# Kernel optimization log

Hardware: AMD Instinct MI355X
Metric: run time of the kernel (lower is better)

Reference implementation:

```python
import math
import jax, jax.numpy as jnp
import numpy as np

L, D, H, F, V, S, B = 6, 1024, 16, 4096, 32000, 1024, 2
DH = D // H


def setup_inputs() -> dict:
    key = jax.random.key(0)
    ks = jax.random.split(key, 24)

    def u(k, shape, fan_in):
        b = 1.0 / math.sqrt(fan_in)
        return jax.random.uniform(k, shape, jnp.float32, -b, b)

    inp = {
        "input_ids": jax.random.randint(ks[0], (B, S), 0, V),
        "attention_mask": jnp.ones((B, 1, 1, S), dtype=bool),
        "emb": jax.random.normal(ks[1], (V, D), jnp.float32),
        "pos": 0.02 * jax.random.normal(ks[2], (1, S, D), jnp.float32),
        "ln1_w": jnp.ones((L, D), jnp.float32),
        "ln1_b": jnp.zeros((L, D), jnp.float32),
        "qw": u(ks[3], (L, D, D), D), "qb": u(ks[4], (L, D), D),
        "kw": u(ks[5], (L, D, D), D), "kb": u(ks[6], (L, D), D),
        "vw": u(ks[7], (L, D, D), D), "vb": u(ks[8], (L, D), D),
        "ow": u(ks[9], (L, D, D), D), "ob": u(ks[10], (L, D), D),
        "ln2_w": jnp.ones((L, D), jnp.float32),
        "ln2_b": jnp.zeros((L, D), jnp.float32),
        "w1": u(ks[11], (L, F, D), D), "b1": u(ks[12], (L, F), D),
        "w2": u(ks[13], (L, D, F), F), "b2": u(ks[14], (L, D), F),
    }
    return inp


def _ln(x, w, b, eps=1e-5):
    m = x.mean(axis=-1, keepdims=True)
    v = ((x - m) ** 2).mean(axis=-1, keepdims=True)  # unbiased=False
    return w * (x - m) / jnp.sqrt(v + eps) + b


def _gelu(x):
    # tanh-approx GELU, exactly as in source
    return 0.5 * x * (1.0 + jnp.tanh(math.sqrt(2.0 / math.pi) * (x + 0.044715 * x ** 3)))


def reference(input_ids, attention_mask, emb, pos, ln1_w, ln1_b,
              qw, qb, kw, kb, vw, vb, ow, ob,
              ln2_w, ln2_b, w1, b1, w2, b2):
    b, s = input_ids.shape
    d = emb.shape[1]
    scale = math.sqrt(DH)
    x = emb[input_ids] * math.sqrt(d) + pos[:, :s, :]  # [B,S,D]
    n_layers = qw.shape[0]
    for l in range(n_layers):
        h = _ln(x, ln1_w[l], ln1_b[l])
        q = (h @ qw[l].T + qb[l]).reshape(b, s, H, DH)
        k = (h @ kw[l].T + kb[l]).reshape(b, s, H, DH)
        v = (h @ vw[l].T + vb[l]).reshape(b, s, H, DH)
        scores = jnp.einsum('bqhd,bkhd->bhqk', q, k) / scale  # [B,H,S,S]
        scores = jnp.where(attention_mask, scores, -jnp.inf)
        attn = jax.nn.softmax(scores, axis=-1)
        o = jnp.einsum('bhqk,bkhd->bqhd', attn, v).reshape(b, s, d)
        x = x + (o @ ow[l].T + ob[l])
        h2 = _ln(x, ln2_w[l], ln2_b[l])
        x = x + (_gelu(h2 @ w1[l].T + b1[l]) @ w2[l].T + b2[l])
    return x
```

## Files before the change

### kernel.cpp

```cpp
#include <hip/hip_runtime.h>
#include <hip/hip_bf16.h>
#include <math.h>

#define D_ 1024
#define H_ 16
#define F_ 4096
#define S_ 1024
#define B_ 2
#define MTOT 2048

using bf16 = __hip_bfloat16;
typedef __bf16 bf16x8 __attribute__((ext_vector_type(8)));
typedef float f32x4 __attribute__((ext_vector_type(4)));

__device__ __forceinline__ void gload_lds16(const void* g, void* l) {
  __builtin_amdgcn_global_load_lds((const __attribute__((address_space(1))) void*)g,
                                   (__attribute__((address_space(3))) void*)l, 16, 0, 0);
}

__device__ __forceinline__ unsigned short f2b(float f) {
  union { bf16 h; unsigned short u; } c;
  c.h = __float2bfloat16(f);
  return c.u;
}

__global__ __launch_bounds__(256) void embed_kernel(const int* __restrict__ ids,
    const float* __restrict__ emb, const float* __restrict__ pos, float* __restrict__ x) {
  int row = blockIdx.x;
  int s = row & (S_ - 1);
  int id = ids[row];
  const float4* e = (const float4*)(emb + (size_t)id * D_);
  const float4* p = (const float4*)(pos + (size_t)s * D_);
  float4* xo = (float4*)(x + (size_t)row * D_);
  int t = threadIdx.x;
  float4 ev = e[t], pv = p[t], r;
  r.x = ev.x * 32.0f + pv.x; r.y = ev.y * 32.0f + pv.y;
  r.z = ev.z * 32.0f + pv.z; r.w = ev.w * 32.0f + pv.w;
  xo[t] = r;
}

__global__ __launch_bounds__(256) void ln_kernel(const float* __restrict__ x,
    const float* __restrict__ w, const float* __restrict__ b, bf16* __restrict__ h) {
  int row = blockIdx.x, t = threadIdx.x;
  const float4* xr = (const float4*)(x + (size_t)row * D_);
  float4 v = xr[t];
  float s = v.x + v.y + v.z + v.w;
  float s2 = v.x * v.x + v.y * v.y + v.z * v.z + v.w * v.w;
  #pragma unroll
  for (int o = 32; o; o >>= 1) { s += __shfl_down(s, o); s2 += __shfl_down(s2, o); }
  __shared__ float red[8];
  int wave = t >> 6, lane = t & 63;
  if (lane == 0) { red[wave] = s; red[4 + wave] = s2; }
  __syncthreads();
  float mean = (red[0] + red[1] + red[2] + red[3]) * (1.0f / D_);
  float m2   = (red[4] + red[5] + red[6] + red[7]) * (1.0f / D_);
  float rstd = rsqrtf(m2 - mean * mean + 1e-5f);
  float4 wv = ((const float4*)w)[t], bv = ((const float4*)b)[t];
  ushort4 o4;
  o4.x = f2b((v.x - mean) * rstd * wv.x + bv.x);
  o4.y = f2b((v.y - mean) * rstd * wv.y + bv.y);
  o4.z = f2b((v.z - mean) * rstd * wv.z + bv.z);
  o4.w = f2b((v.w - mean) * rstd * wv.w + bv.w);
  ((ushort4*)(h + (size_t)row * D_))[t] = o4;
}

__global__ __launch_bounds__(256) void cvt6_kernel(const float4* __restrict__ s0,
    const float4* __restrict__ s1, const float4* __restrict__ s2, const float4* __restrict__ s3,
    const float4* __restrict__ s4, const float4* __restrict__ s5, ushort4* __restrict__ dst) {
  int i = blockIdx.x * 256 + threadIdx.x;
  const float4* src; int off;
  if (i < 1048576) {
    int seg = i >> 18; off = i & 262143;
    src = seg == 0 ? s0 : seg == 1 ? s1 : seg == 2 ? s2 : s3;
  } else if (i < 2097152) { src = s4; off = i - 1048576; }
  else                    { src = s5; off = i - 2097152; }
  float4 v = src[off];
  ushort4 r;
  r.x = f2b(v.x); r.y = f2b(v.y); r.z = f2b(v.z); r.w = f2b(v.w);
  dst[i] = r;
}

template<int MODE>
__global__ __launch_bounds__(256) void gemm_bt(const bf16* __restrict__ A,
    const bf16* __restrict__ Bw,
    const float* __restrict__ b0_, const float* __restrict__ b1_, const float* __restrict__ b2_,
    void* __restrict__ o0, void* __restrict__ o1, void* __restrict__ o2,
    int M, int N, int K, int kspl) {
  __shared__ alignas(16) bf16 As[2][128 * 64];
  __shared__ alignas(16) bf16 Bs[2][128 * 64];
  int tid = threadIdx.x, wave = tid >> 6, lane = tid & 63;
  int nbn = N >> 7;
  int nwg = gridDim.x;
  int bid = blockIdx.x;
  int swz = (bid & 7) * (nwg >> 3) + (bid >> 3);
  int bm = swz / nbn, bn = swz % nbn;
  int m0 = bm << 7, n0 = bn << 7;
  int kbase = blockIdx.z * kspl;
  int wr = wave >> 1, wc = wave & 1;
  int lr = lane & 15, lg = lane >> 4;

  auto stage = [&](int buf, int k0) {
    #pragma unroll
    for (int j = 0; j < 4; j++) {
      int cidx = j * 256 + tid;
      int r = cidx >> 3, s = cidx & 7;
      int g = s ^ (r & 7);
      bf16* abase = &As[buf][(j * 256 + wave * 64) * 8];
      bf16* bbase = &Bs[buf][(j * 256 + wave * 64) * 8];
      gload_lds16(A  + (size_t)(m0 + r) * K + k0 + g * 8, abase);
      gload_lds16(Bw + (size_t)(n0 + r) * K + k0 + g * 8, bbase);
    }
  };

  f32x4 acc[4][4] = {};
  int nk = kspl >> 6;
  stage(0, kbase);
  __syncthreads();
  int cur = 0;
  for (int t = 0; t < nk; ++t) {
    if (t + 1 < nk) stage(cur ^ 1, kbase + (t + 1) * 64);
    __builtin_amdgcn_s_setprio(1);
    #pragma unroll
    for (int kk = 0; kk < 2; ++kk) {
      bf16x8 af[4], bfr[4];
      #pragma unroll
      for (int f = 0; f < 4; f++) {
        int ra = wr * 64 + f * 16 + lr;
        int rb = wc * 64 + f * 16 + lr;
        af[f]  = *(const bf16x8*)&As[cur][ra * 64 + (((kk * 4 + lg) ^ (ra & 7)) * 8)];
        bfr[f] = *(const bf16x8*)&Bs[cur][rb * 64 + (((kk * 4 + lg) ^ (rb & 7)) * 8)];
      }
      #pragma unroll
      for (int mf = 0; mf < 4; mf++)
        #pragma unroll
        for (int nf = 0; nf < 4; nf++)
          acc[mf][nf] = __builtin_amdgcn_mfma_f32_16x16x32_bf16(af[mf], bfr[nf], acc[mf][nf], 0, 0, 0);
    }
    __builtin_amdgcn_s_setprio(0);
    __syncthreads();
    cur ^= 1;
  }

  #pragma unroll
  for (int mf = 0; mf < 4; mf++) {
    #pragma unroll
    for (int nf = 0; nf < 4; nf++) {
      int n = n0 + wc * 64 + nf * 16 + lr;
      if (MODE == 0 && n >= 2048) {
        int nl = n & 1023;
        int mbase = m0 + wr * 64 + mf * 16 + lg * 4;
        int bb = mbase >> 10, sb = mbase & 1023;
        float bias = b2_[nl];
        ushort4 pk;
        pk.x = f2b(acc[mf][nf][0] + bias);
        pk.y = f2b(acc[mf][nf][1] + bias);
        pk.z = f2b(acc[mf][nf][2] + bias);
        pk.w = f2b(acc[mf][nf][3] + bias);
        *(ushort4*)&((bf16*)o2)[((size_t)(bb * 1024 + nl)) * 1024 + sb] = pk;
      } else {
        #pragma unroll
        for (int i = 0; i < 4; i++) {
          int m = m0 + wr * 64 + mf * 16 + lg * 4 + i;
          float v = acc[mf][nf][i];
          if (MODE == 0) {
            int seg = n >> 10, nl = n & 1023;
            if (seg == 0)      ((bf16*)o0)[(size_t)m * 1024 + nl] = __float2bfloat16(v + b0_[nl]);
            else               ((bf16*)o1)[(size_t)m * 1024 + nl] = __float2bfloat16(v + b1_[nl]);
          } else if (MODE == 1) {
            float bias = (blockIdx.z == 0) ? b0_[n] : 0.0f;
            atomicAdd(&((float*)o0)[(size_t)m * N + n], v + bias);
          } else {
            float g = v + b0_[n];
            float t = tanhf(0.7978845608028654f * (g + 0.044715f * g * g * g));
            ((bf16*)o0)[(size_t)m * N + n] = __float2bfloat16(0.5f * g * (1.0f + t));
          }
        }
      }
    }
  }
}

__global__ __launch_bounds__(256) void attn_kernel(const bf16* __restrict__ qbuf,
    const bf16* __restrict__ kbuf, const bf16* __restrict__ vT, bf16* __restrict__ obuf) {
  int bh = blockIdx.y;
  int b = bh >> 4, h = bh & 15;
  int q0 = blockIdx.x * 16;
  int tid = threadIdx.x, wave = tid >> 6, lane = tid & 63;
  int lr = lane & 15, lg = lane >> 4;

  __shared__ alignas(16) bf16 P[16][1032];
  __shared__ float red[4][16];

  const bf16* qp = qbuf + ((size_t)(b * S_ + q0)) * D_ + h * 64;
  bf16x8 aq[2];
  aq[0] = *(const bf16x8*)(qp + (size_t)lr * D_ + lg * 8);
  aq[1] = *(const bf16x8*)(qp + (size_t)lr * D_ + 32 + lg * 8);

  const bf16* kb_ = kbuf + ((size_t)(b * S_)) * D_ + h * 64;
  int nbase = wave * 256;
  f32x4 acc[16] = {};
  #pragma unroll
  for (int nf = 0; nf < 16; nf++) {
    const bf16* kp = kb_ + (size_t)(nbase + nf * 16 + lr) * D_ + lg * 8;
    bf16x8 bk0 = *(const bf16x8*)(kp);
    bf16x8 bk1 = *(const bf16x8*)(kp + 32);
    acc[nf] = __builtin_amdgcn_mfma_f32_16x16x32_bf16(aq[0], bk0, acc[nf], 0, 0, 0);
    acc[nf] = __builtin_amdgcn_mfma_f32_16x16x32_bf16(aq[1], bk1, acc[nf], 0, 0, 0);
  }

  float pm[4];
  #pragma unroll
  for (int i = 0; i < 4; i++) {
    float m = acc[0][i];
    #pragma unroll
    for (int nf = 1; nf < 16; nf++) m = fmaxf(m, acc[nf][i]);
    pm[i] = m;
  }
  #pragma unroll
  for (int msk = 1; msk < 16; msk <<= 1)
    #pragma unroll
    for (int i = 0; i < 4; i++) pm[i] = fmaxf(pm[i], __shfl_xor(pm[i], msk));
  if (lr == 0)
    #pragma unroll
    for (int i = 0; i < 4; i++) red[wave][lg * 4 + i] = pm[i];
  __syncthreads();

  float gm[4];
  #pragma unroll
  for (int i = 0; i < 4; i++) {
    int r = lg * 4 + i;
    gm[i] = fmaxf(fmaxf(red[0][r], red[1][r]), fmaxf(red[2][r], red[3][r]));
  }

  float ps[4] = {0.f, 0.f, 0.f, 0.f};
  #pragma unroll
  for (int nf = 0; nf < 16; nf++)
    #pragma unroll
    for (int i = 0; i < 4; i++) {
      float p = __expf((acc[nf][i] - gm[i]) * 0.125f);
      ps[i] += p;
      P[lg * 4 + i][nbase + nf * 16 + lr] = __float2bfloat16(p);
    }
  #pragma unroll
  for (int msk = 1; msk < 16; msk <<= 1)
    #pragma unroll
    for (int i = 0; i < 4; i++) ps[i] += __shfl_xor(ps[i], msk);
  __syncthreads();
  if (lr == 0)
    #pragma unroll
    for (int i = 0; i < 4; i++) red[wave][lg * 4 + i] = ps[i];
  __syncthreads();
  float rs[4];
  #pragma unroll
  for (int i = 0; i < 4; i++) {
    int r = lg * 4 + i;
    rs[i] = red[0][r] + red[1][r] + red[2][r] + red[3][r];
  }

  const bf16* vp = vT + ((size_t)(b * D_ + h * 64 + wave * 16 + lr)) * S_ + lg * 8;
  f32x4 oacc = {};
  #pragma unroll 8
  for (int k0 = 0; k0 < S_; k0 += 32) {
    bf16x8 pa = *(const bf16x8*)&P[lr][k0 + lg * 8];
    bf16x8 bv = *(const bf16x8*)(vp + k0);
    oacc = __builtin_amdgcn_mfma_f32_16x16x32_bf16(pa, bv, oacc, 0, 0, 0);
  }
  #pragma unroll
  for (int i = 0; i < 4; i++) {
    int r = lg * 4 + i;
    obuf[((size_t)(b * S_ + q0 + r)) * D_ + h * 64 + wave * 16 + lr] =
        __float2bfloat16(oacc[i] / rs[i]);
  }
}

extern "C" void kernel_launch(void* const* d_in, const int* in_sizes, int n_in,
                              void* d_out, int out_size, void* d_ws, size_t ws_size,
                              hipStream_t stream) {
  const int*   ids  = (const int*)d_in[0];
  const float* emb  = (const float*)d_in[2];
  const float* pos  = (const float*)d_in[3];
  const float* ln1w = (const float*)d_in[4];
  const float* ln1b = (const float*)d_in[5];
  const float* qw = (const float*)d_in[6];  const float* qb = (const float*)d_in[7];
  const float* kw = (const float*)d_in[8];  const float* kb = (const float*)d_in[9];
  const float* vw = (const float*)d_in[10]; const float* vb = (const float*)d_in[11];
  const float* ow = (const float*)d_in[12]; const float* ob = (const float*)d_in[13];
  const float* ln2w = (const float*)d_in[14]; const float* ln2b = (const float*)d_in[15];
  const float* w1 = (const float*)d_in[16]; const float* b1 = (const float*)d_in[17];
  const float* w2 = (const float*)d_in[18]; const float* b2 = (const float*)d_in[19];
  (void)in_sizes; (void)n_in; (void)out_size; (void)ws_size;

  float* x = (float*)d_out;
  char* ws = (char*)d_ws;
  const size_t SZ_ACT = (size_t)MTOT * D_ * 2;
  bf16* h    = (bf16*)(ws);
  bf16* q    = (bf16*)(ws + SZ_ACT);
  bf16* k    = (bf16*)(ws + 2 * SZ_ACT);
  bf16* vt   = (bf16*)(ws + 3 * SZ_ACT);
  bf16* o    = (bf16*)(ws + 4 * SZ_ACT);
  bf16* mid  = (bf16*)(ws + 5 * SZ_ACT);
  bf16* wbuf = (bf16*)(ws + 5 * SZ_ACT + (size_t)MTOT * F_ * 2);

  const size_t DD = (size_t)D_ * D_;
  const size_t FD = (size_t)F_ * D_;

  embed_kernel<<<MTOT, 256, 0, stream>>>(ids, emb, pos, x);

  for (int l = 0; l < 6; l++) {
    cvt6_kernel<<<12288, 256, 0, stream>>>(
        (const float4*)(qw + l * DD), (const float4*)(kw + l * DD),
        (const float4*)(vw + l * DD), (const float4*)(ow + l * DD),
        (const float4*)(w1 + l * FD), (const float4*)(w2 + l * FD),
        (ushort4*)wbuf);

    ln_kernel<<<MTOT, 256, 0, stream>>>(x, ln1w + l * D_, ln1b + l * D_, h);

    gemm_bt<0><<<dim3(384, 1, 1), 256, 0, stream>>>(h, wbuf,
        qb + l * D_, kb + l * D_, vb + l * D_, q, k, vt, MTOT, 3072, 1024, 1024);

    attn_kernel<<<dim3(64, 32), 256, 0, stream>>>(q, k, vt, o);

    gemm_bt<1><<<dim3(128, 1, 2), 256, 0, stream>>>(o, wbuf + 3 * DD,
        ob + l * D_, nullptr, nullptr, x, nullptr, nullptr, MTOT, 1024, 1024, 512);

    ln_kernel<<<MTOT, 256, 0, stream>>>(x, ln2w + l * D_, ln2b + l * D_, h);

    gemm_bt<2><<<dim3(512, 1, 1), 256, 0, stream>>>(h, wbuf + 4 * DD,
        b1 + l * F_, nullptr, nullptr, mid, nullptr, nullptr, MTOT, 4096, 1024, 1024);

    gemm_bt<1><<<dim3(128, 1, 2), 256, 0, stream>>>(mid, wbuf + 4 * DD + FD,
        b2 + l * D_, nullptr, nullptr, x, nullptr, nullptr, MTOT, 1024, 4096, 2048);
  }
}
```

Baseline: 1.237 ms.

## Batch weight conversion, replace split-K atomics with 64-row triple-buffered GEMM tiles

All six layers' weights are now converted to bf16 in one launch before the layer loop, replacing six per-layer conversion kernels. The output-projection and FFN-down GEMMs drop split-K with atomicAdd and instead use 64-row M tiles with a three-stage LDS pipeline driven by explicit vmcnt waits, so results go out with a plain read-modify-write. GELU switches from tanhf to an algebraically equivalent exp-based sigmoid form, and the attention MFMA loops are wrapped in s_setprio. The trade-offs are a larger workspace holding every layer's weights, fewer K-parallel workgroups, and hand-tuned wait counts that depend on the number of loads issued per stage.

```diff
diff --git a/kernel.cpp b/kernel.cpp
--- a/kernel.cpp
+++ b/kernel.cpp
@@ -64,115 +64,150 @@
   ((ushort4*)(h + (size_t)row * D_))[t] = o4;
 }
 
-__global__ __launch_bounds__(256) void cvt6_kernel(const float4* __restrict__ s0,
-    const float4* __restrict__ s1, const float4* __restrict__ s2, const float4* __restrict__ s3,
-    const float4* __restrict__ s4, const float4* __restrict__ s5, ushort4* __restrict__ dst) {
+__global__ __launch_bounds__(256) void cvt_all_kernel(const float4* __restrict__ qw,
+    const float4* __restrict__ kw, const float4* __restrict__ vw, const float4* __restrict__ ow,
+    const float4* __restrict__ w1, const float4* __restrict__ w2, ushort4* __restrict__ dst) {
   int i = blockIdx.x * 256 + threadIdx.x;
+  int layer = i / 3145728;
+  int r = i - layer * 3145728;
   const float4* src; int off;
-  if (i < 1048576) {
-    int seg = i >> 18; off = i & 262143;
-    src = seg == 0 ? s0 : seg == 1 ? s1 : seg == 2 ? s2 : s3;
-  } else if (i < 2097152) { src = s4; off = i - 1048576; }
-  else                    { src = s5; off = i - 2097152; }
+  if (r < 1048576) {
+    int seg = r >> 18; off = (r & 262143) + layer * 262144;
+    src = seg == 0 ? qw : seg == 1 ? kw : seg == 2 ? vw : ow;
+  } else if (r < 2097152) { src = w1; off = (r - 1048576) + layer * 1048576; }
+  else                    { src = w2; off = (r - 2097152) + layer * 1048576; }
   float4 v = src[off];
-  ushort4 r;
-  r.x = f2b(v.x); r.y = f2b(v.y); r.z = f2b(v.z); r.w = f2b(v.w);
-  dst[i] = r;
-}
-
-template<int MODE>
+  ushort4 p;
+  p.x = f2b(v.x); p.y = f2b(v.y); p.z = f2b(v.z); p.w = f2b(v.w);
+  dst[i] = p;
+}
+
+template<int MODE, int TM>
 __global__ __launch_bounds__(256) void gemm_bt(const bf16* __restrict__ A,
     const bf16* __restrict__ Bw,
     const float* __restrict__ b0_, const float* __restrict__ b1_, const float* __restrict__ b2_,
     void* __restrict__ o0, void* __restrict__ o1, void* __restrict__ o2,
-    int M, int N, int K, int kspl) {
-  __shared__ alignas(16) bf16 As[2][128 * 64];
-  __shared__ alignas(16) bf16 Bs[2][128 * 64];
+    int M, int N, int K) {
+  constexpr int NBUF = (TM == 128) ? 2 : 3;
+  constexpr int FA   = TM / 32;
+  __shared__ alignas(16) bf16 As[NBUF][TM * 64];
+  __shared__ alignas(16) bf16 Bs[NBUF][128 * 64];
   int tid = threadIdx.x, wave = tid >> 6, lane = tid & 63;
-  int nbn = N >> 7;
+  int nbm = M / TM;
   int nwg = gridDim.x;
   int bid = blockIdx.x;
   int swz = (bid & 7) * (nwg >> 3) + (bid >> 3);
-  int bm = swz / nbn, bn = swz % nbn;
-  int m0 = bm << 7, n0 = bn << 7;
-  int kbase = blockIdx.z * kspl;
+  int bm = swz % nbm, bn = swz / nbm;
+  int m0 = bm * TM, n0 = bn << 7;
   int wr = wave >> 1, wc = wave & 1;
   int lr = lane & 15, lg = lane >> 4;
 
   auto stage = [&](int buf, int k0) {
+    #pragma unroll
+    for (int j = 0; j < TM / 32; j++) {
+      int cidx = j * 256 + tid;
+      int r = cidx >> 3, s = cidx & 7;
+      int g = s ^ (r & 7);
+      gload_lds16(A + (size_t)(m0 + r) * K + k0 + g * 8, &As[buf][(j * 256 + wave * 64) * 8]);
+    }
     #pragma unroll
     for (int j = 0; j < 4; j++) {
       int cidx = j * 256 + tid;
       int r = cidx >> 3, s = cidx & 7;
       int g = s ^ (r & 7);
-      bf16* abase = &As[buf][(j * 256 + wave * 64) * 8];
-      bf16* bbase = &Bs[buf][(j * 256 + wave * 64) * 8];
-      gload_lds16(A  + (size_t)(m0 + r) * K + k0 + g * 8, abase);
-      gload_lds16(Bw + (size_t)(n0 + r) * K + k0 + g * 8, bbase);
+      gload_lds16(Bw + (size_t)(n0 + r) * K + k0 + g * 8, &Bs[buf][(j * 256 + wave * 64) * 8]);
     }
   };
 
-  f32x4 acc[4][4] = {};
-  int nk = kspl >> 6;
-  stage(0, kbase);
-  __syncthreads();
-  int cur = 0;
-  for (int t = 0; t < nk; ++t) {
-    if (t + 1 < nk) stage(cur ^ 1, kbase + (t + 1) * 64);
-    __builtin_amdgcn_s_setprio(1);
+  auto mfma_tile = [&](int buf, f32x4 (&acc)[FA][4]) {
     #pragma unroll
     for (int kk = 0; kk < 2; ++kk) {
-      bf16x8 af[4], bfr[4];
+      bf16x8 af[FA], bfr[4];
+      #pragma unroll
+      for (int f = 0; f < FA; f++) {
+        int ra = wr * (TM / 2) + f * 16 + lr;
+        af[f] = *(const bf16x8*)&As[buf][ra * 64 + (((kk * 4 + lg) ^ (ra & 7)) * 8)];
+      }
       #pragma unroll
       for (int f = 0; f < 4; f++) {
-        int ra = wr * 64 + f * 16 + lr;
         int rb = wc * 64 + f * 16 + lr;
-        af[f]  = *(const bf16x8*)&As[cur][ra * 64 + (((kk * 4 + lg) ^ (ra & 7)) * 8)];
-        bfr[f] = *(const bf16x8*)&Bs[cur][rb * 64 + (((kk * 4 + lg) ^ (rb & 7)) * 8)];
+        bfr[f] = *(const bf16x8*)&Bs[buf][rb * 64 + (((kk * 4 + lg) ^ (rb & 7)) * 8)];
       }
       #pragma unroll
-      for (int mf = 0; mf < 4; mf++)
+      for (int mf = 0; mf < FA; mf++)
         #pragma unroll
         for (int nf = 0; nf < 4; nf++)
           acc[mf][nf] = __builtin_amdgcn_mfma_f32_16x16x32_bf16(af[mf], bfr[nf], acc[mf][nf], 0, 0, 0);
     }
-    __builtin_amdgcn_s_setprio(0);
+  };
+
+  f32x4 acc[FA][4] = {};
+  int nk = K >> 6;
+
+  if constexpr (TM == 128) {
+    stage(0, 0);
     __syncthreads();
-    cur ^= 1;
-  }
-
-  #pragma unroll
-  for (int mf = 0; mf < 4; mf++) {
+    int cur = 0;
+    for (int t = 0; t < nk; ++t) {
+      if (t + 1 < nk) stage(cur ^ 1, (t + 1) * 64);
+      __builtin_amdgcn_s_setprio(1);
+      mfma_tile(cur, acc);
+      __builtin_amdgcn_s_setprio(0);
+      __syncthreads();
+      cur ^= 1;
+    }
+  } else {
+    stage(0, 0);
+    stage(1, 64);
+    int rb = 0;
+    for (int t = 0; t < nk; ++t) {
+      int sb = rb + 2; if (sb >= 3) sb -= 3;
+      if (t + 2 < nk) stage(sb, (t + 2) * 64);
+      if (t + 2 < nk)      asm volatile("s_waitcnt vmcnt(12)" ::: "memory");
+      else if (t + 1 < nk) asm volatile("s_waitcnt vmcnt(6)"  ::: "memory");
+      else                 asm volatile("s_waitcnt vmcnt(0)"  ::: "memory");
+      __builtin_amdgcn_s_barrier();
+      __builtin_amdgcn_sched_barrier(0);
+      __builtin_amdgcn_s_setprio(1);
+      mfma_tile(rb, acc);
+      __builtin_amdgcn_s_setprio(0);
+      __builtin_amdgcn_s_barrier();
+      rb += 1; if (rb >= 3) rb -= 3;
+    }
+  }
+
+  #pragma unroll
+  for (int mf = 0; mf < FA; mf++) {
     #pragma unroll
     for (int nf = 0; nf < 4; nf++) {
       int n = n0 + wc * 64 + nf * 16 + lr;
       if (MODE == 0 && n >= 2048) {
         int nl = n & 1023;
-        int mbase = m0 + wr * 64 + mf * 16 + lg * 4;
-        int bb = mbase >> 10, sb = mbase & 1023;
+        int mbase = m0 + wr * (TM / 2) + mf * 16 + lg * 4;
+        int bb = mbase >> 10, sb2 = mbase & 1023;
         float bias = b2_[nl];
         ushort4 pk;
         pk.x = f2b(acc[mf][nf][0] + bias);
         pk.y = f2b(acc[mf][nf][1] + bias);
         pk.z = f2b(acc[mf][nf][2] + bias);
         pk.w = f2b(acc[mf][nf][3] + bias);
-        *(ushort4*)&((bf16*)o2)[((size_t)(bb * 1024 + nl)) * 1024 + sb] = pk;
+        *(ushort4*)&((bf16*)o2)[((size_t)(bb * 1024 + nl)) * 1024 + sb2] = pk;
       } else {
         #pragma unroll
         for (int i = 0; i < 4; i++) {
-          int m = m0 + wr * 64 + mf * 16 + lg * 4 + i;
+          int m = m0 + wr * (TM / 2) + mf * 16 + lg * 4 + i;
           float v = acc[mf][nf][i];
           if (MODE == 0) {
             int seg = n >> 10, nl = n & 1023;
             if (seg == 0)      ((bf16*)o0)[(size_t)m * 1024 + nl] = __float2bfloat16(v + b0_[nl]);
             else               ((bf16*)o1)[(size_t)m * 1024 + nl] = __float2bfloat16(v + b1_[nl]);
           } else if (MODE == 1) {
-            float bias = (blockIdx.z == 0) ? b0_[n] : 0.0f;
-            atomicAdd(&((float*)o0)[(size_t)m * N + n], v + bias);
+            float* xp = (float*)o0;
+            xp[(size_t)m * N + n] += v + b0_[n];
           } else {
             float g = v + b0_[n];
-            float t = tanhf(0.7978845608028654f * (g + 0.044715f * g * g * g));
-            ((bf16*)o0)[(size_t)m * N + n] = __float2bfloat16(0.5f * g * (1.0f + t));
+            float e = __expf(-1.5957691216057308f * (g + 0.044715f * g * g * g));
+            ((bf16*)o0)[(size_t)m * N + n] = __float2bfloat16(g / (1.0f + e));
           }
         }
       }
@@ -199,6 +234,7 @@
   const bf16* kb_ = kbuf + ((size_t)(b * S_)) * D_ + h * 64;
   int nbase = wave * 256;
   f32x4 acc[16] = {};
+  __builtin_amdgcn_s_setprio(1);
   #pragma unroll
   for (int nf = 0; nf < 16; nf++) {
     const bf16* kp = kb_ + (size_t)(nbase + nf * 16 + lr) * D_ + lg * 8;
@@ -207,6 +243,7 @@
     acc[nf] = __builtin_amdgcn_mfma_f32_16x16x32_bf16(aq[0], bk0, acc[nf], 0, 0, 0);
     acc[nf] = __builtin_amdgcn_mfma_f32_16x16x32_bf16(aq[1], bk1, acc[nf], 0, 0, 0);
   }
+  __builtin_amdgcn_s_setprio(0);
 
   float pm[4];
   #pragma unroll
@@ -259,12 +296,14 @@
 
   const bf16* vp = vT + ((size_t)(b * D_ + h * 64 + wave * 16 + lr)) * S_ + lg * 8;
   f32x4 oacc = {};
+  __builtin_amdgcn_s_setprio(1);
   #pragma unroll 8
   for (int k0 = 0; k0 < S_; k0 += 32) {
     bf16x8 pa = *(const bf16x8*)&P[lr][k0 + lg * 8];
     bf16x8 bv = *(const bf16x8*)(vp + k0);
     oacc = __builtin_amdgcn_mfma_f32_16x16x32_bf16(pa, bv, oacc, 0, 0, 0);
   }
+  __builtin_amdgcn_s_setprio(0);
   #pragma unroll
   for (int i = 0; i < 4; i++) {
     int r = lg * 4 + i;
@@ -303,32 +342,33 @@
 
   const size_t DD = (size_t)D_ * D_;
   const size_t FD = (size_t)F_ * D_;
+  const size_t WL = 4 * DD + 2 * FD;
+
+  cvt_all_kernel<<<73728, 256, 0, stream>>>(
+      (const float4*)qw, (const float4*)kw, (const float4*)vw, (const float4*)ow,
+      (const float4*)w1, (const float4*)w2, (ushort4*)wbuf);
 
   embed_kernel<<<MTOT, 256, 0, stream>>>(ids, emb, pos, x);
 
   for (int l = 0; l < 6; l++) {
-    cvt6_kernel<<<12288, 256, 0, stream>>>(
-        (const float4*)(qw + l * DD), (const float4*)(kw + l * DD),
-        (const float4*)(vw + l * DD), (const float4*)(ow + l * DD),
-        (const float4*)(w1 + l * FD), (const float4*)(w2 + l * FD),
-        (ushort4*)wbuf);
+    bf16* wl = wbuf + (size_t)l * WL;
 
     ln_kernel<<<MTOT, 256, 0, stream>>>(x, ln1w + l * D_, ln1b + l * D_, h);
 
-    gemm_bt<0><<<dim3(384, 1, 1), 256, 0, stream>>>(h, wbuf,
-        qb + l * D_, kb + l * D_, vb + l * D_, q, k, vt, MTOT, 3072, 1024, 1024);
+    gemm_bt<0, 128><<<dim3(384, 1, 1), 256, 0, stream>>>(h, wl,
+        qb + l * D_, kb + l * D_, vb + l * D_, q, k, vt, MTOT, 3072, 1024);
 
     attn_kernel<<<dim3(64, 32), 256, 0, stream>>>(q, k, vt, o);
 
-    gemm_bt<1><<<dim3(128, 1, 2), 256, 0, stream>>>(o, wbuf + 3 * DD,
-        ob + l * D_, nullptr, nullptr, x, nullptr, nullptr, MTOT, 1024, 1024, 512);
+    gemm_bt<1, 64><<<dim3(256, 1, 1), 256, 0, stream>>>(o, wl + 3 * DD,
+        ob + l * D_, nullptr, nullptr, x, nullptr, nullptr, MTOT, 1024, 1024);
 
     ln_kernel<<<MTOT, 256, 0, stream>>>(x, ln2w + l * D_, ln2b + l * D_, h);
 
-    gemm_bt<2><<<dim3(512, 1, 1), 256, 0, stream>>>(h, wbuf + 4 * DD,
-        b1 + l * F_, nullptr, nullptr, mid, nullptr, nullptr, MTOT, 4096, 1024, 1024);
-
-    gemm_bt<1><<<dim3(128, 1, 2), 256, 0, stream>>>(mid, wbuf + 4 * DD + FD,
-        b2 + l * D_, nullptr, nullptr, x, nullptr, nullptr, MTOT, 1024, 4096, 2048);
-  }
-}
+    gemm_bt<2, 128><<<dim3(512, 1, 1), 256, 0, stream>>>(h, wl + 4 * DD,
+        b1 + l * F_, nullptr, nullptr, mid, nullptr, nullptr, MTOT, 4096, 1024);
+
+    gemm_bt<1, 64><<<dim3(256, 1, 1), 256, 0, stream>>>(mid, wl + 4 * DD + FD,
+        b2 + l * D_, nullptr, nullptr, x, nullptr, nullptr, MTOT, 1024, 4096);
+  }
+}
```

Measured after the change: 1.468 ms. 1.19x slower.

## Batch weight conversion, use exp-based GELU, raise split-K, prioritize attention MFMA

Applied to the files above, without the earlier changes.

Converts all layers' weights to bf16 in a single grid-stride kernel before the layer loop, instead of one launch per layer, storing each layer in its own slice of the workspace. GELU is rewritten as x*sigmoid(2z) using a fast exp in place of tanhf. Split-K for the output projection and FFN down-projection doubles from 2 to 4 to fill more CUs. The trade-off is more atomics, and the workspace now has to hold six layers of bf16 weights. The attention MFMA loops are wrapped in s_setprio hints.

```diff
diff --git a/kernel.cpp b/kernel.cpp
--- a/kernel.cpp
+++ b/kernel.cpp
@@ -64,20 +64,25 @@
   ((ushort4*)(h + (size_t)row * D_))[t] = o4;
 }
 
-__global__ __launch_bounds__(256) void cvt6_kernel(const float4* __restrict__ s0,
-    const float4* __restrict__ s1, const float4* __restrict__ s2, const float4* __restrict__ s3,
-    const float4* __restrict__ s4, const float4* __restrict__ s5, ushort4* __restrict__ dst) {
-  int i = blockIdx.x * 256 + threadIdx.x;
-  const float4* src; int off;
-  if (i < 1048576) {
-    int seg = i >> 18; off = i & 262143;
-    src = seg == 0 ? s0 : seg == 1 ? s1 : seg == 2 ? s2 : s3;
-  } else if (i < 2097152) { src = s4; off = i - 1048576; }
-  else                    { src = s5; off = i - 2097152; }
-  float4 v = src[off];
-  ushort4 r;
-  r.x = f2b(v.x); r.y = f2b(v.y); r.z = f2b(v.z); r.w = f2b(v.w);
-  dst[i] = r;
+__global__ __launch_bounds__(256) void cvt_all_kernel(const float4* __restrict__ qw,
+    const float4* __restrict__ kw, const float4* __restrict__ vw, const float4* __restrict__ ow,
+    const float4* __restrict__ w1, const float4* __restrict__ w2, ushort4* __restrict__ dst) {
+  const int total = 18874368;
+  int stride = gridDim.x * 256;
+  for (int i = blockIdx.x * 256 + threadIdx.x; i < total; i += stride) {
+    int layer = i / 3145728;
+    int r = i - layer * 3145728;
+    const float4* src; int off;
+    if (r < 1048576) {
+      int seg = r >> 18; off = (r & 262143) + layer * 262144;
+      src = seg == 0 ? qw : seg == 1 ? kw : seg == 2 ? vw : ow;
+    } else if (r < 2097152) { src = w1; off = (r - 1048576) + layer * 1048576; }
+    else                    { src = w2; off = (r - 2097152) + layer * 1048576; }
+    float4 v = src[off];
+    ushort4 p;
+    p.x = f2b(v.x); p.y = f2b(v.y); p.z = f2b(v.z); p.w = f2b(v.w);
+    dst[i] = p;
+  }
 }
 
 template<int MODE>
@@ -171,8 +176,8 @@
             atomicAdd(&((float*)o0)[(size_t)m * N + n], v + bias);
           } else {
             float g = v + b0_[n];
-            float t = tanhf(0.7978845608028654f * (g + 0.044715f * g * g * g));
-            ((bf16*)o0)[(size_t)m * N + n] = __float2bfloat16(0.5f * g * (1.0f + t));
+            float e = __expf(-1.5957691216057308f * (g + 0.044715f * g * g * g));
+            ((bf16*)o0)[(size_t)m * N + n] = __float2bfloat16(g / (1.0f + e));
           }
         }
       }
@@ -199,6 +204,7 @@
   const bf16* kb_ = kbuf + ((size_t)(b * S_)) * D_ + h * 64;
   int nbase = wave * 256;
   f32x4 acc[16] = {};
+  __builtin_amdgcn_s_setprio(1);
   #pragma unroll
   for (int nf = 0; nf < 16; nf++) {
     const bf16* kp = kb_ + (size_t)(nbase + nf * 16 + lr) * D_ + lg * 8;
@@ -207,6 +213,7 @@
     acc[nf] = __builtin_amdgcn_mfma_f32_16x16x32_bf16(aq[0], bk0, acc[nf], 0, 0, 0);
     acc[nf] = __builtin_amdgcn_mfma_f32_16x16x32_bf16(aq[1], bk1, acc[nf], 0, 0, 0);
   }
+  __builtin_amdgcn_s_setprio(0);
 
   float pm[4];
   #pragma unroll
@@ -259,12 +266,14 @@
 
   const bf16* vp = vT + ((size_t)(b * D_ + h * 64 + wave * 16 + lr)) * S_ + lg * 8;
   f32x4 oacc = {};
+  __builtin_amdgcn_s_setprio(1);
   #pragma unroll 8
   for (int k0 = 0; k0 < S_; k0 += 32) {
     bf16x8 pa = *(const bf16x8*)&P[lr][k0 + lg * 8];
     bf16x8 bv = *(const bf16x8*)(vp + k0);
     oacc = __builtin_amdgcn_mfma_f32_16x16x32_bf16(pa, bv, oacc, 0, 0, 0);
   }
+  __builtin_amdgcn_s_setprio(0);
   #pragma unroll
   for (int i = 0; i < 4; i++) {
     int r = lg * 4 + i;
@@ -303,32 +312,33 @@
 
   const size_t DD = (size_t)D_ * D_;
   const size_t FD = (size_t)F_ * D_;
+  const size_t WL = 4 * DD + 2 * FD;
+
+  cvt_all_kernel<<<2048, 256, 0, stream>>>(
+      (const float4*)qw, (const float4*)kw, (const float4*)vw, (const float4*)ow,
+      (const float4*)w1, (const float4*)w2, (ushort4*)wbuf);
 
   embed_kernel<<<MTOT, 256, 0, stream>>>(ids, emb, pos, x);
 
   for (int l = 0; l < 6; l++) {
-    cvt6_kernel<<<12288, 256, 0, stream>>>(
-        (const float4*)(qw + l * DD), (const float4*)(kw + l * DD),
-        (const float4*)(vw + l * DD), (const float4*)(ow + l * DD),
-        (const float4*)(w1 + l * FD), (const float4*)(w2 + l * FD),
-        (ushort4*)wbuf);
+    bf16* wl = wbuf + (size_t)l * WL;
 
     ln_kernel<<<MTOT, 256, 0, stream>>>(x, ln1w + l * D_, ln1b + l * D_, h);
 
-    gemm_bt<0><<<dim3(384, 1, 1), 256, 0, stream>>>(h, wbuf,
+    gemm_bt<0><<<dim3(384, 1, 1), 256, 0, stream>>>(h, wl,
         qb + l * D_, kb + l * D_, vb + l * D_, q, k, vt, MTOT, 3072, 1024, 1024);
 
     attn_kernel<<<dim3(64, 32), 256, 0, stream>>>(q, k, vt, o);
 
-    gemm_bt<1><<<dim3(128, 1, 2), 256, 0, stream>>>(o, wbuf + 3 * DD,
-        ob + l * D_, nullptr, nullptr, x, nullptr, nullptr, MTOT, 1024, 1024, 512);
+    gemm_bt<1><<<dim3(128, 1, 4), 256, 0, stream>>>(o, wl + 3 * DD,
+        ob + l * D_, nullptr, nullptr, x, nullptr, nullptr, MTOT, 1024, 1024, 256);
 
     ln_kernel<<<MTOT, 256, 0, stream>>>(x, ln2w + l * D_, ln2b + l * D_, h);
 
-    gemm_bt<2><<<dim3(512, 1, 1), 256, 0, stream>>>(h, wbuf + 4 * DD,
+    gemm_bt<2><<<dim3(512, 1, 1), 256, 0, stream>>>(h, wl + 4 * DD,
         b1 + l * F_, nullptr, nullptr, mid, nullptr, nullptr, MTOT, 4096, 1024, 1024);
 
-    gemm_bt<1><<<dim3(128, 1, 2), 256, 0, stream>>>(mid, wbuf + 4 * DD + FD,
-        b2 + l * D_, nullptr, nullptr, x, nullptr, nullptr, MTOT, 1024, 4096, 2048);
-  }
-}
+    gemm_bt<1><<<dim3(128, 1, 4), 256, 0, stream>>>(mid, wl + 4 * DD + FD,
+        b2 + l * D_, nullptr, nullptr, x, nullptr, nullptr, MTOT, 1024, 4096, 1024);
+  }
+}
```

After: 1.341 ms. 8.3% more time.
